# Kernel optimization log

Hardware: AMD Instinct MI355X
Metric: run time of the kernel (lower is better)

## Reference

```python
import jax, jax.numpy as jnp
import numpy as np

N_U, N_I, D_IN_U, D_IN_I, D, D_QOL, B = 4096, 4096, 256, 256, 256, 4, 8192

def _w(key, shape, scale=0.05):
    return (jax.random.normal(key, shape) * scale).astype(jnp.float32)

def setup_inputs() -> dict:
    key = jax.random.key(0)
    ks = jax.random.split(key, 24)
    inp = {
        "x_u": jax.random.normal(ks[0], (N_U, D_IN_U), jnp.float32),
        "x_i": jax.random.normal(ks[1], (N_I, D_IN_I), jnp.float32),
        "social_adj": jax.random.randint(ks[2], (N_U, N_U), 0, 2, jnp.int32),
        "ui_adj": jax.random.randint(ks[3], (N_U, N_I), 0, 2, jnp.int32),
        "user_idx": jax.random.randint(ks[4], (B,), 0, N_U, jnp.int32),
        "item_idx": jax.random.randint(ks[5], (B,), 0, N_I, jnp.int32),
        "q_u": jax.random.normal(ks[6], (N_U, D_QOL), jnp.float32),
        # params (Linear stored as [in, out]; y = x @ W + b)
        "user_W": _w(ks[7], (D_IN_U, D)), "user_b": jnp.zeros((D,), jnp.float32),
        "item_W": _w(ks[8], (D_IN_I, D)), "item_b": jnp.zeros((D,), jnp.float32),
        "soc_W": _w(ks[9], (D, D)), "soc_a": _w(ks[10], (2 * D,)),
        "cnt_W": _w(ks[11], (D, D)), "cnt_a": _w(ks[12], (2 * D,)),
        "gate_W": _w(ks[13], (D_QOL, D)), "gate_b": jnp.zeros((D,), jnp.float32),
        "qproj_W": _w(ks[14], (D_QOL, D)), "qproj_b": jnp.zeros((D,), jnp.float32),
        "alpha_q": jnp.float32(0.3),
        "pred_W1": _w(ks[15], (2 * D, D)), "pred_b1": jnp.zeros((D,), jnp.float32),
        "pred_W2": _w(ks[16], (D, 1)), "pred_b2": jnp.zeros((1,), jnp.float32),
    }
    return inp

def _gat(Wh_src, Wh_dst, a, adj):
    """GAT additive attention: src rows attend over dst cols where adj!=0.
    Rows with no neighbors produce zero output (matches nan_to_num + zeroing)."""
    d = Wh_src.shape[-1]
    a1 = Wh_src @ a[:d]          # [N_src]
    a2 = Wh_dst @ a[d:]          # [N_dst]
    e = jax.nn.leaky_relu(a1[:, None] + a2[None, :], 0.2)  # [N_src, N_dst]
    mask = adj != 0
    neg_inf = jnp.float32(-jnp.inf)
    m = jnp.max(jnp.where(mask, e, neg_inf), axis=-1, keepdims=True)
    m = jnp.where(jnp.isfinite(m), m, 0.0)  # guard empty rows
    ex = jnp.where(mask, jnp.exp(e - m), 0.0)
    denom = jnp.sum(ex, axis=-1, keepdims=True)
    alpha = jnp.where(denom > 0, ex / jnp.where(denom > 0, denom, 1.0), 0.0)
    out = alpha @ Wh_dst
    return out, alpha

def reference(x_u, x_i, social_adj, ui_adj, user_idx, item_idx, q_u,
              user_W, user_b, item_W, item_b, soc_W, soc_a, cnt_W, cnt_a,
              gate_W, gate_b, qproj_W, qproj_b, alpha_q,
              pred_W1, pred_b1, pred_W2, pred_b2):
    h_u = x_u @ user_W + user_b               # [N_u, D]
    h_i = x_i @ item_W + item_b               # [N_i, D]
    # social attention (users over users)
    Wh = h_u @ soc_W
    soc_msg, alpha_s = _gat(Wh, Wh, soc_a, social_adj)
    # content attention (users over items)
    Wu = h_u @ cnt_W
    Wi = h_i @ cnt_W
    cnt_msg, alpha_c = _gat(Wu, Wi, cnt_a, ui_adj)
    h_u_out = jax.nn.elu(soc_msg + cnt_msg + h_u)
    # QoL gate
    gate = jax.nn.sigmoid(q_u @ gate_W + gate_b)
    qproj = q_u @ qproj_W + qproj_b
    h_u_out = h_u_out + alpha_q * gate * qproj
    # pair prediction (dropout inactive at eval)
    cat = jnp.concatenate([h_u_out[user_idx], h_i[item_idx]], axis=-1)  # [B, 2D]
    hid = jax.nn.relu(cat @ pred_W1 + pred_b1)
    r = (hid @ pred_W2 + pred_b2)[..., 0]
    r_hat = 1.0 + 4.0 * jax.nn.sigmoid(r)
    return r_hat, alpha_s, alpha_c
```

## Files before the change

### kernel.cpp

```cpp
#include <hip/hip_runtime.h>

typedef unsigned short u16;
typedef unsigned int u32;
typedef unsigned char u8;
typedef unsigned long long u64;
typedef float f32x4 __attribute__((ext_vector_type(4)));
typedef int i32x4 __attribute__((ext_vector_type(4)));
typedef __bf16 bf16x8 __attribute__((ext_vector_type(8)));

#define NU 4096
#define DD 256
#define BB 8192

__device__ inline u16 f2b(float f) {
    u32 u = __builtin_bit_cast(u32, f);
    u32 r = (u + 0x7fffu + ((u >> 16) & 1u)) >> 16;
    return (u16)r;
}
__device__ inline float b2f(u16 v) { return __builtin_bit_cast(float, (u32)v << 16); }
__device__ inline float lrelu(float x) { return x > 0.f ? x : 0.2f * x; }
__device__ inline float decmax(u32 e) {
    return __builtin_bit_cast(float, (e >> 31) ? (e & 0x7fffffffu) : ~e);
}

#define BARRIER_LGKM() asm volatile("s_waitcnt lgkmcnt(0)\ns_barrier" ::: "memory")

__global__ __launch_bounds__(256) void k_pro(
    const float* __restrict__ x_u, const float* __restrict__ x_i,
    const float* __restrict__ user_W, const float* __restrict__ item_W, const float* __restrict__ pred_W1,
    const float* __restrict__ soc_W, const float* __restrict__ soc_a,
    const float* __restrict__ cnt_W, const float* __restrict__ cnt_a,
    const float* __restrict__ user_b, const float* __restrict__ item_b,
    u16* __restrict__ xu_b, u16* __restrict__ xi_b,
    u16* __restrict__ uWt, u16* __restrict__ iWt, u16* __restrict__ p1Wt,
    float* __restrict__ uvec,
    u16* __restrict__ WusT, u16* __restrict__ WicT,
    float* __restrict__ b_us, float* __restrict__ b_ic, u32* __restrict__ MhEnc) {
    __shared__ float t[64][65];
    __shared__ float sa[256];
    const int b = blockIdx.x;
    const int tid = threadIdx.x;

    if (b < 1024) {
        const float* in = (b < 512) ? x_u : x_i;
        u16* out = (b < 512) ? xu_b : xi_b;
        int i = (b & 511) * 256 + tid;
        const float4 v0 = *(const float4*)(in + (size_t)i * 8);
        const float4 v1 = *(const float4*)(in + (size_t)i * 8 + 4);
        u16 u[8] = {f2b(v0.x), f2b(v0.y), f2b(v0.z), f2b(v0.w),
                    f2b(v1.x), f2b(v1.y), f2b(v1.z), f2b(v1.w)};
        *(uint4*)(out + (size_t)i * 8) = *(uint4*)u;
    } else if (b < 1088) {
        int j = b - 1024;
        const float* in;
        u16* out;
        int R;
        if (j < 16) { in = user_W; out = uWt; R = 256; }
        else if (j < 32) { in = item_W; out = iWt; R = 256; j -= 16; }
        else { in = pred_W1; out = p1Wt; R = 512; j -= 32; }
        int rb = (j >> 2) * 64, cb = (j & 3) * 64;
        for (int k = 0; k < 16; ++k) {
            int idx = k * 256 + tid;
            int lr = idx >> 6, lc = idx & 63;
            t[lr][lc] = in[(size_t)(rb + lr) * 256 + cb + lc];
        }
        __syncthreads();
        for (int k = 0; k < 16; ++k) {
            int idx = k * 256 + tid;
            int lr = idx >> 6, lc = idx & 63;
            out[(size_t)(cb + lr) * R + rb + lc] = f2b(t[lc][lr]);
        }
    } else if (b < 1092) {
        int bb = b - 1088;
        if (bb == 0 && tid < 2) MhEnc[tid] = 0u;
        const float* W = (bb < 2) ? soc_W : cnt_W;
        const float* a = ((bb < 2) ? soc_a : cnt_a) + (bb & 1) * 256;
        int lane = tid & 63, wv = tid >> 6;
        sa[tid] = a[tid];
        __syncthreads();
        for (int rr = 0; rr < 64; ++rr) {
            int in = wv * 64 + rr;
            float4 w4 = *(const float4*)(W + (size_t)in * 256 + lane * 4);
            float acc = w4.x * sa[lane * 4] + w4.y * sa[lane * 4 + 1] + w4.z * sa[lane * 4 + 2] + w4.w * sa[lane * 4 + 3];
#pragma unroll
            for (int off = 32; off; off >>= 1) acc += __shfl_down(acc, off);
            if (lane == 0) uvec[bb * 256 + in] = acc;
        }
    } else {
        int j = b - 1092;
        int p = j >> 4;
        int tile = j & 15;
        const float* A = p ? item_W : user_W;
        const float* Bw = p ? cnt_W : soc_W;
        const float* bvec = p ? item_b : user_b;
        u16* outT = p ? WicT : WusT;
        float* outb = p ? b_ic : b_us;
        int m0 = (tile >> 2) * 64, n0 = (tile & 3) * 64;
        int m = m0 + (tid >> 4) * 4, n = n0 + (tid & 15) * 4;
        float acc[4][4];
#pragma unroll
        for (int i = 0; i < 4; ++i)
#pragma unroll
            for (int k = 0; k < 4; ++k) acc[i][k] = 0.f;
        for (int k0 = 0; k0 < 256; k0 += 4) {
            float aa[4][4], bb2[4][4];
#pragma unroll
            for (int i = 0; i < 4; ++i) {
                float4 v = *(const float4*)(A + (size_t)(m + i) * 256 + k0);
                aa[i][0] = v.x; aa[i][1] = v.y; aa[i][2] = v.z; aa[i][3] = v.w;
            }
#pragma unroll
            for (int k = 0; k < 4; ++k) {
                float4 v = *(const float4*)(Bw + (size_t)(k0 + k) * 256 + n);
                bb2[k][0] = v.x; bb2[k][1] = v.y; bb2[k][2] = v.z; bb2[k][3] = v.w;
            }
#pragma unroll
            for (int i = 0; i < 4; ++i)
#pragma unroll
                for (int k = 0; k < 4; ++k)
#pragma unroll
                    for (int jj = 0; jj < 4; ++jj) acc[i][jj] += aa[i][k] * bb2[k][jj];
        }
#pragma unroll
        for (int i = 0; i < 4; ++i)
#pragma unroll
            for (int jj = 0; jj < 4; ++jj) outT[(size_t)(n + jj) * 256 + m + i] = f2b(acc[i][jj]);
        if (tile >> 2 == 0 && tid < 64) {
            int nn = n0 + tid;
            float s = 0.f;
            for (int k = 0; k < 256; ++k) s += bvec[k] * Bw[(size_t)k * 256 + nn];
            outb[nn] = s;
        }
    }
}

__global__ __launch_bounds__(256) void k_gemm4(
    const u16* __restrict__ xu_b, const u16* __restrict__ xi_b,
    const u16* __restrict__ uWt, const u16* __restrict__ iWt,
    const u16* __restrict__ WusT, const u16* __restrict__ WicT,
    const float* __restrict__ user_b, const float* __restrict__ item_b,
    const float* __restrict__ b_us, const float* __restrict__ b_ic,
    float* __restrict__ h_u_f, float* __restrict__ h_i_f, u16* __restrict__ h_i_b,
    u16* __restrict__ WhT, u16* __restrict__ WiT) {
    const int z = blockIdx.z;
    const int M = 4096, N = 256, K = 256;
    const u16* A = (z == 0 || z == 2) ? xu_b : xi_b;
    const u16* Bt = (z == 0) ? uWt : (z == 1) ? iWt : (z == 2) ? WusT : WicT;
    const float* bias = (z == 0) ? user_b : (z == 1) ? item_b : (z == 2) ? b_us : b_ic;
    float* Cf = (z == 0) ? h_u_f : (z == 1) ? h_i_f : nullptr;
    u16* Cb = (z == 1) ? h_i_b : nullptr;
    u16* Cbt = (z == 2) ? WhT : (z == 3) ? WiT : nullptr;

    __shared__ u16 As[64 * 64];
    __shared__ u16 Bs[64 * 64];
    const int tid = threadIdx.x;
    const int lane = tid & 63, wv = tid >> 6;
    const int bm = blockIdx.x * 64, bn = blockIdx.y * 64;
    const int wm = (wv >> 1) * 32, wn = (wv & 1) * 32;
    f32x4 acc[2][2];
#pragma unroll
    for (int i = 0; i < 2; i++)
#pragma unroll
        for (int j = 0; j < 2; j++) acc[i][j] = f32x4{0.f, 0.f, 0.f, 0.f};

    char* Ab = (char*)As;
    char* Bb = (char*)Bs;
    const int r = tid >> 2;
    const int ib0 = (tid & 3) * 32;
    const int swz = (r & 7) << 4;

    for (int k0 = 0; k0 < K; k0 += 64) {
        const uint4* ga = (const uint4*)(A + (size_t)(bm + r) * K + k0 + (ib0 >> 1));
        const uint4* gb = (const uint4*)(Bt + (size_t)(bn + r) * K + k0 + (ib0 >> 1));
        uint4 va0 = ga[0], va1 = ga[1];
        uint4 vb0 = gb[0], vb1 = gb[1];
        __syncthreads();
        *(uint4*)(Ab + r * 128 + ((ib0) ^ swz)) = va0;
        *(uint4*)(Ab + r * 128 + ((ib0 + 16) ^ swz)) = va1;
        *(uint4*)(Bb + r * 128 + ((ib0) ^ swz)) = vb0;
        *(uint4*)(Bb + r * 128 + ((ib0 + 16) ^ swz)) = vb1;
        __syncthreads();
#pragma unroll
        for (int kh = 0; kh < 2; ++kh) {
            bf16x8 af[2], bfr[2];
#pragma unroll
            for (int mf = 0; mf < 2; ++mf) {
                int row = wm + mf * 16 + (lane & 15);
                int kb = kh * 64 + ((lane >> 4) << 4);
                af[mf] = *(const bf16x8*)(Ab + row * 128 + (kb ^ ((row & 7) << 4)));
            }
#pragma unroll
            for (int nf = 0; nf < 2; ++nf) {
                int row = wn + nf * 16 + (lane & 15);
                int kb = kh * 64 + ((lane >> 4) << 4);
                bfr[nf] = *(const bf16x8*)(Bb + row * 128 + (kb ^ ((row & 7) << 4)));
            }
#pragma unroll
            for (int mf = 0; mf < 2; ++mf)
#pragma unroll
                for (int nf = 0; nf < 2; ++nf)
                    acc[mf][nf] = __builtin_amdgcn_mfma_f32_16x16x32_bf16(af[mf], bfr[nf], acc[mf][nf], 0, 0, 0);
        }
    }
#pragma unroll
    for (int mf = 0; mf < 2; ++mf) {
#pragma unroll
        for (int nf = 0; nf < 2; ++nf) {
            int col = bn + wn + nf * 16 + (lane & 15);
            int row0 = bm + wm + mf * 16 + ((lane >> 4) << 2);
            float bv = bias[col];
            float v[4];
#pragma unroll
            for (int q = 0; q < 4; ++q) {
                float x = acc[mf][nf][q] + bv;
                v[q] = x;
                if (Cf) Cf[(size_t)(row0 + q) * N + col] = x;
                if (Cb) Cb[(size_t)(row0 + q) * N + col] = f2b(x);
            }
            if (Cbt) {
                uint2 p;
                p.x = (u32)f2b(v[0]) | ((u32)f2b(v[1]) << 16);
                p.y = (u32)f2b(v[2]) | ((u32)f2b(v[3]) << 16);
                *(uint2*)(Cbt + (size_t)col * M + row0) = p;
            }
        }
    }
}

__global__ __launch_bounds__(256) void k_gemv_a(const float* __restrict__ h_u, const float* __restrict__ h_i,
                                                const float* __restrict__ uvec, float* __restrict__ avec,
                                                u32* __restrict__ MhEnc) {
    int tid = threadIdx.x, lane = tid & 63, wv = tid >> 6;
    int ib = blockIdx.x * 64;
    const float* H = (wv == 3) ? h_i : h_u;
    const float* u = uvec + wv * 256;
    float4 u4 = *(const float4*)(u + lane * 4);
    float runm = -1e30f;
    for (int rr = 0; rr < 64; ++rr) {
        int row = ib + rr;
        float4 h4 = *(const float4*)(H + (size_t)row * 256 + lane * 4);
        float acc = h4.x * u4.x + h4.y * u4.y + h4.z * u4.z + h4.w * u4.w;
#pragma unroll
        for (int off = 32; off; off >>= 1) acc += __shfl_down(acc, off);
        if (lane == 0) {
            avec[wv * 4096 + row] = acc;
            runm = fmaxf(runm, acc);
        }
    }
    if (lane == 0 && (wv & 1)) {
        u32 b = __builtin_bit_cast(u32, runm);
        u32 e = (b >> 31) ? ~b : (b | 0x80000000u);
        atomicMax(&MhEnc[wv >> 1], e);
    }
}

__global__ __launch_bounds__(512) void k_scan(const int* __restrict__ adjS, const int* __restrict__ adjC,
                                              u8* __restrict__ bits) {
    const int z = blockIdx.z;
    const int* adj = z ? adjC : adjS;
    u8* bz = bits + (size_t)z * 2097152;
    const int lane = threadIdx.x & 63, wv = threadIdx.x >> 6;
    const int row = blockIdx.x * 8 + wv;
    const int* base = adj + (size_t)row * 4096 + lane * 8;
    i32x4 va[8], vb[8];
#pragma unroll
    for (int s = 0; s < 8; ++s) {
        va[s] = __builtin_nontemporal_load((const i32x4*)(base + s * 512));
        vb[s] = __builtin_nontemporal_load((const i32x4*)(base + s * 512 + 4));
    }
    const size_t bo = (size_t)row * 512 + lane;
#pragma unroll
    for (int s = 0; s < 8; ++s) {
        i32x4 v0 = va[s], v1 = vb[s];
        u32 b = (u32)(v0.x != 0) | ((u32)(v0.y != 0) << 1) | ((u32)(v0.z != 0) << 2) | ((u32)(v0.w != 0) << 3) |
                ((u32)(v1.x != 0) << 4) | ((u32)(v1.y != 0) << 5) | ((u32)(v1.z != 0) << 6) | ((u32)(v1.w != 0) << 7);
        bz[bo + s * 64] = (u8)b;
    }
}

__global__ __launch_bounds__(512, 4) void k_pv(const u8* __restrict__ bits,
                                               const float* __restrict__ avec, const u32* __restrict__ MhEnc,
                                               const u16* __restrict__ WhT, const u16* __restrict__ WiT,
                                               float* __restrict__ dpart, u16* __restrict__ msgpart) {
    const int z = blockIdx.z;
    const int ib = blockIdx.x * 64;
    const int jb = blockIdx.y * 512;
    const int tid = threadIdx.x, lane = tid & 63, wv = tid >> 6;
    const u8* bz = bits + (size_t)z * 2097152;
    const float* a1 = avec + z * 8192;
    const float* a2 = a1 + 4096;
    const u16* Pt = z ? WiT : WhT;

    __shared__ float a2s[512];
    __shared__ float s_a1[64], s_mr[64];
    __shared__ u16 Atile[64 * 512];
    char* Ab = (char*)Atile;

    if (tid < 512) a2s[tid] = a2[jb + tid];
    if (tid < 64) {
        float a = a1[ib + tid];
        float mhg = decmax(MhEnc[z]);
        s_a1[tid] = a;
        s_mr[tid] = lrelu(a + mhg);
    }
    __syncthreads();

    const int r0 = wv * 8;
    u8 bvv[8];
    const size_t bo = (size_t)(ib + r0) * 512 + (jb >> 3) + lane;
#pragma unroll
    for (int rr = 0; rr < 8; ++rr) bvv[rr] = bz[bo + (size_t)rr * 512];
    const float4 A0 = *(const float4*)(a2s + lane * 8);
    const float4 A1 = *(const float4*)(a2s + lane * 8 + 4);
    const float av[8] = {A0.x, A0.y, A0.z, A0.w, A1.x, A1.y, A1.z, A1.w};
#pragma unroll
    for (int rr = 0; rr < 8; ++rr) {
        const int r = r0 + rr;
        const float a1r = s_a1[r], mr = s_mr[r];
        const u32 byte = bvv[rr];
        float ex[8];
        float acc = 0.f;
#pragma unroll
        for (int k = 0; k < 8; ++k) {
            float e = __expf(lrelu(a1r + av[k]) - mr);
            ex[k] = ((byte >> k) & 1) ? e : 0.f;
            acc += ex[k];
        }
#pragma unroll
        for (int off = 32; off; off >>= 1) acc += __shfl_down(acc, off);
        if (lane == 0) dpart[((size_t)z * 8 + blockIdx.y) * 4096 + ib + r] = acc;
        u16 pk[8];
#pragma unroll
        for (int k = 0; k < 8; ++k) pk[k] = f2b(ex[k]);
        *(uint4*)(Ab + r * 1024 + ((lane * 16) ^ ((r & 7) << 4))) = *(uint4*)pk;
    }
    BARRIER_LGKM();

    f32x4 acc[4][2];
#pragma unroll
    for (int i = 0; i < 4; i++)
#pragma unroll
        for (int j = 0; j < 2; j++) acc[i][j] = f32x4{0.f, 0.f, 0.f, 0.f};

    const u16* pts = Pt + (size_t)(wv * 32 + (lane & 15)) * 4096 + jb + ((lane >> 4) << 3);
    bf16x8 bcur0 = *(const bf16x8*)(pts);
    bf16x8 bcur1 = *(const bf16x8*)(pts + (size_t)16 * 4096);
    for (int ks = 0; ks < 16; ++ks) {
        bf16x8 bnxt0, bnxt1;
        if (ks < 15) {
            bnxt0 = *(const bf16x8*)(pts + (ks + 1) * 32);
            bnxt1 = *(const bf16x8*)(pts + (size_t)16 * 4096 + (ks + 1) * 32);
        }
#pragma unroll
        for (int mf = 0; mf < 4; ++mf) {
            int ra = mf * 16 + (lane & 15);
            bf16x8 af = *(const bf16x8*)(Ab + ra * 1024 + ((ks * 64 + ((lane >> 4) << 4)) ^ ((ra & 7) << 4)));
            acc[mf][0] = __builtin_amdgcn_mfma_f32_16x16x32_bf16(af, bcur0, acc[mf][0], 0, 0, 0);
            acc[mf][1] = __builtin_amdgcn_mfma_f32_16x16x32_bf16(af, bcur1, acc[mf][1], 0, 0, 0);
        }
        bcur0 = bnxt0;
        bcur1 = bnxt1;
    }

    u16* mp = msgpart + ((size_t)(z * 8 + blockIdx.y) * 4096 + ib) * 256;
#pragma unroll
    for (int mf = 0; mf < 4; ++mf) {
        int rr = mf * 16 + ((lane >> 4) << 2);
#pragma unroll
        for (int nf = 0; nf < 2; ++nf) {
            int col = wv * 32 + nf * 16 + (lane & 15);
#pragma unroll
            for (int q = 0; q < 4; ++q) mp[(size_t)(rr + q) * 256 + col] = f2b(acc[mf][nf][q]);
        }
    }
}

__global__ __launch_bounds__(256) void k_alpha(const u8* __restrict__ bits,
                                               const float* __restrict__ avec, const u32* __restrict__ MhEnc,
                                               const float* __restrict__ dpart, float* __restrict__ out) {
    const int z = blockIdx.z;
    const int ib = blockIdx.x * 16;
    const int tid = threadIdx.x, lane = tid & 63, wv = tid >> 6;
    const u8* bz = bits + (size_t)z * 2097152;
    const float* a1 = avec + z * 8192;
    const float* a2 = a1 + 4096;
    float* alpha = out + 8192 + (size_t)z * 16777216;

    __shared__ float a2s[4096];
    __shared__ u8 bls[16 * 512];
    __shared__ float s_a1[16], s_mr[16], s_inv[16];

#pragma unroll
    for (int k = 0; k < 4; ++k)
        *(float4*)(a2s + (k * 256 + tid) * 4) = *(const float4*)(a2 + (k * 256 + tid) * 4);
#pragma unroll
    for (int k = 0; k < 2; ++k)
        *(uint4*)(bls + (k * 256 + tid) * 16) = *(const uint4*)(bz + (size_t)ib * 512 + (k * 256 + tid) * 16);
    if (tid < 16) {
        float a = a1[ib + tid];
        float mhg = decmax(MhEnc[z]);
        s_a1[tid] = a;
        s_mr[tid] = lrelu(a + mhg);
        float d = 0.f;
#pragma unroll
        for (int s = 0; s < 8; ++s) d += dpart[((size_t)(z * 8 + s)) * 4096 + ib + tid];
        s_inv[tid] = d > 0.f ? 1.f / d : 0.f;
    }
    __syncthreads();

    const int bsub = lane >> 1;
    const int sh = (lane & 1) * 4;
#pragma unroll
    for (int rr = 0; rr < 4; ++rr) {
        const int r = wv * 4 + rr;
        const int row = ib + r;
        const float a1r = s_a1[r], mr = s_mr[r], ivr = s_inv[r];
        float* ap = alpha + (size_t)row * 4096;
        const u8* brow = bls + r * 512;
#pragma unroll
        for (int c = 0; c < 16; ++c) {
            const int col = c * 256 + lane * 4;
            const u32 nib = ((u32)brow[c * 32 + bsub]) >> sh;
            const float4 a4 = *(const float4*)(a2s + col);
            f32x4 o;
            o.x = (nib & 1) ? __expf(lrelu(a1r + a4.x) - mr) * ivr : 0.f;
            o.y = (nib & 2) ? __expf(lrelu(a1r + a4.y) - mr) * ivr : 0.f;
            o.z = (nib & 4) ? __expf(lrelu(a1r + a4.z) - mr) * ivr : 0.f;
            o.w = (nib & 8) ? __expf(lrelu(a1r + a4.w) - mr) * ivr : 0.f;
            __builtin_nontemporal_store(o, (f32x4*)(ap + col));
        }
    }
}

__global__ __launch_bounds__(256) void k_post(const u16* __restrict__ msgpart, const float* __restrict__ dpart,
                                              const float* __restrict__ h_u, const float* __restrict__ q_u,
                                              const float* __restrict__ gate_W, const float* __restrict__ gate_b,
                                              const float* __restrict__ qproj_W, const float* __restrict__ qproj_b,
                                              const float* __restrict__ alpha_q, u16* __restrict__ huo_b) {
    int i = blockIdx.x;
    int n = threadIdx.x;
    __shared__ float red[16];
    if (n < 16) red[n] = dpart[(size_t)n * 4096 + i];
    __syncthreads();
    float d0 = 0.f, d1 = 0.f;
#pragma unroll
    for (int p = 0; p < 8; ++p) { d0 += red[p]; d1 += red[8 + p]; }
    float inv0 = d0 > 0.f ? 1.f / d0 : 0.f;
    float inv1 = d1 > 0.f ? 1.f / d1 : 0.f;
    float s0 = 0.f, s1 = 0.f;
#pragma unroll
    for (int p = 0; p < 8; ++p) {
        s0 += b2f(msgpart[((size_t)p * 4096 + i) * 256 + n]);
        s1 += b2f(msgpart[((size_t)(8 + p) * 4096 + i) * 256 + n]);
    }
    float v = inv0 * s0 + inv1 * s1 + h_u[(size_t)i * 256 + n];
    v = v > 0.f ? v : expm1f(v);
    float q0 = q_u[i * 4 + 0], q1 = q_u[i * 4 + 1], q2 = q_u[i * 4 + 2], q3 = q_u[i * 4 + 3];
    float g = q0 * gate_W[n] + q1 * gate_W[256 + n] + q2 * gate_W[512 + n] + q3 * gate_W[768 + n] + gate_b[n];
    g = 1.f / (1.f + __expf(-g));
    float qp = q0 * qproj_W[n] + q1 * qproj_W[256 + n] + q2 * qproj_W[512 + n] + q3 * qproj_W[768 + n] + qproj_b[n];
    float o = v + alpha_q[0] * g * qp;
    huo_b[(size_t)i * 256 + n] = f2b(o);
}

__global__ __launch_bounds__(512) void k_pred(const u16* __restrict__ huo_b, const u16* __restrict__ h_i_b,
                                              const int* __restrict__ uidx, const int* __restrict__ iidx,
                                              const u16* __restrict__ Bt, const float* __restrict__ b1,
                                              const float* __restrict__ W2, const float* __restrict__ b2,
                                              float* __restrict__ out) {
    __shared__ u16 As[64 * 512];
    __shared__ float redL[512];
    const int tid = threadIdx.x, lane = tid & 63, wv = tid >> 6;
    const int bm = blockIdx.x * 64;
    char* Ab = (char*)As;

    {
        const int r = tid >> 3;
        const int uix = uidx[bm + r], iix = iidx[bm + r];
        const int sswz = (r & 7) << 4;
#pragma unroll
        for (int c = 0; c < 8; ++c) {
            int e = c * 64 + (tid & 7) * 8;
            const u16* src = (e < 256) ? (huo_b + (size_t)uix * 256 + e) : (h_i_b + (size_t)iix * 256 + (e - 256));
            uint4 v = *(const uint4*)src;
            *(uint4*)(Ab + r * 1024 + ((e * 2) ^ sswz)) = v;
        }
    }
    __syncthreads();

    const int n0 = wv * 32;
    f32x4 acc[4][2];
#pragma unroll
    for (int i = 0; i < 4; i++)
#pragma unroll
        for (int j = 0; j < 2; j++) acc[i][j] = f32x4{0.f, 0.f, 0.f, 0.f};

    for (int ks = 0; ks < 16; ++ks) {
        bf16x8 bfr[2];
#pragma unroll
        for (int nf = 0; nf < 2; ++nf)
            bfr[nf] = *(const bf16x8*)(Bt + (size_t)(n0 + nf * 16 + (lane & 15)) * 512 + ks * 32 + ((lane >> 4) << 3));
#pragma unroll
        for (int mf = 0; mf < 4; ++mf) {
            int ra = mf * 16 + (lane & 15);
            bf16x8 af = *(const bf16x8*)(Ab + ra * 1024 + ((ks * 64 + ((lane >> 4) << 4)) ^ ((ra & 7) << 4)));
#pragma unroll
            for (int nf = 0; nf < 2; ++nf)
                acc[mf][nf] = __builtin_amdgcn_mfma_f32_16x16x32_bf16(af, bfr[nf], acc[mf][nf], 0, 0, 0);
        }
    }

    float b1v[2], w2v[2];
#pragma unroll
    for (int nf = 0; nf < 2; ++nf) {
        int col = n0 + nf * 16 + (lane & 15);
        b1v[nf] = b1[col];
        w2v[nf] = W2[col];
    }
#pragma unroll
    for (int mf = 0; mf < 4; ++mf) {
#pragma unroll
        for (int q = 0; q < 4; ++q) {
            float val = 0.f;
#pragma unroll
            for (int nf = 0; nf < 2; ++nf) val += fmaxf(acc[mf][nf][q] + b1v[nf], 0.f) * w2v[nf];
#pragma unroll
            for (int off = 1; off < 16; off <<= 1) val += __shfl_xor(val, off);
            if ((lane & 15) == 0) redL[wv * 64 + mf * 16 + ((lane >> 4) << 2) + q] = val;
        }
    }
    __syncthreads();
    if (tid < 64) {
        float r = b2[0];
#pragma unroll
        for (int w = 0; w < 8; ++w) r += redL[w * 64 + tid];
        out[bm + tid] = 1.f + 4.f / (1.f + __expf(-r));
    }
}

extern "C" void kernel_launch(void* const* d_in, const int* in_sizes, int n_in,
                              void* d_out, int out_size, void* d_ws, size_t ws_size,
                              hipStream_t stream) {
    const float* x_u = (const float*)d_in[0];
    const float* x_i = (const float*)d_in[1];
    const int* adjS = (const int*)d_in[2];
    const int* adjC = (const int*)d_in[3];
    const int* uidx = (const int*)d_in[4];
    const int* iidx = (const int*)d_in[5];
    const float* q_u = (const float*)d_in[6];
    const float* user_W = (const float*)d_in[7];
    const float* user_b = (const float*)d_in[8];
    const float* item_W = (const float*)d_in[9];
    const float* item_b = (const float*)d_in[10];
    const float* soc_W = (const float*)d_in[11];
    const float* soc_a = (const float*)d_in[12];
    const float* cnt_W = (const float*)d_in[13];
    const float* cnt_a = (const float*)d_in[14];
    const float* gate_W = (const float*)d_in[15];
    const float* gate_b = (const float*)d_in[16];
    const float* qproj_W = (const float*)d_in[17];
    const float* qproj_b = (const float*)d_in[18];
    const float* alpha_q = (const float*)d_in[19];
    const float* pred_W1 = (const float*)d_in[20];
    const float* pred_b1 = (const float*)d_in[21];
    const float* pred_W2 = (const float*)d_in[22];
    const float* pred_b2 = (const float*)d_in[23];
    float* out = (float*)d_out;

    char* w = (char*)d_ws;
    size_t off = 0;
    auto alloc = [&](size_t bytes) -> void* {
        void* p = w + off;
        off = (off + bytes + 255) & ~(size_t)255;
        return p;
    };
    u16* xu_b = (u16*)alloc((size_t)NU * DD * 2);
    u16* xi_b = (u16*)alloc((size_t)NU * DD * 2);
    u16* uWt = (u16*)alloc(256 * 256 * 2);
    u16* iWt = (u16*)alloc(256 * 256 * 2);
    u16* p1Wt = (u16*)alloc(512 * 256 * 2);
    u16* WusT = (u16*)alloc(256 * 256 * 2);
    u16* WicT = (u16*)alloc(256 * 256 * 2);
    float* b_us = (float*)alloc(256 * 4);
    float* b_ic = (float*)alloc(256 * 4);
    float* uvec = (float*)alloc(4 * 256 * 4);
    float* h_u_f = (float*)alloc((size_t)NU * DD * 4);
    float* h_i_f = (float*)alloc((size_t)NU * DD * 4);
    u16* h_i_b = (u16*)alloc((size_t)NU * DD * 2);
    u16* WhT = (u16*)alloc((size_t)NU * DD * 2);
    u16* WiT = (u16*)alloc((size_t)NU * DD * 2);
    float* avec = (float*)alloc(4 * 4096 * 4);
    u32* MhEnc = (u32*)alloc(2 * 4);
    float* dpart = (float*)alloc((size_t)2 * 8 * 4096 * 4);
    u8* bits = (u8*)alloc((size_t)2 * 2097152);
    u16* msgpart = (u16*)alloc((size_t)16 * 4096 * 256 * 2);
    u16* huo_b = (u16*)alloc((size_t)NU * DD * 2);
    (void)in_sizes; (void)n_in; (void)out_size; (void)ws_size;

    k_scan<<<dim3(512, 1, 2), 512, 0, stream>>>(adjS, adjC, bits);
    k_pro<<<1124, 256, 0, stream>>>(x_u, x_i, user_W, item_W, pred_W1, soc_W, soc_a, cnt_W, cnt_a,
                                    user_b, item_b, xu_b, xi_b, uWt, iWt, p1Wt, uvec, WusT, WicT,
                                    b_us, b_ic, MhEnc);
    k_gemm4<<<dim3(64, 4, 4), 256, 0, stream>>>(xu_b, xi_b, uWt, iWt, WusT, WicT, user_b, item_b, b_us, b_ic,
                                                h_u_f, h_i_f, h_i_b, WhT, WiT);
    k_gemv_a<<<64, 256, 0, stream>>>(h_u_f, h_i_f, uvec, avec, MhEnc);
    k_pv<<<dim3(64, 8, 2), 512, 0, stream>>>(bits, avec, MhEnc, WhT, WiT, dpart, msgpart);
    k_alpha<<<dim3(256, 1, 2), 256, 0, stream>>>(bits, avec, MhEnc, dpart, out);
    k_post<<<4096, 256, 0, stream>>>(msgpart, dpart, h_u_f, q_u, gate_W, gate_b, qproj_W, qproj_b, alpha_q, huo_b);
    k_pred<<<128, 512, 0, stream>>>(huo_b, h_i_b, uidx, iidx, p1Wt, pred_b1, pred_W2, pred_b2, out);
}
```

Baseline: 192.7 us.

## Fuse adjacency scan with softmax denominator and alpha output writing

Moves the adjacency scan after the attention-logit gemv and fuses it with computing each row's softmax denominator and writing the full alpha matrices. The separate k_alpha kernel and the per-partition denominator buffer in k_pv are removed. This saves a re-read of the bitmask and a kernel launch, and drops the denominator reduction from k_pv. In exchange, each wave computes the exponentials twice per row. The adjacency read no longer overlaps the prologue and GEMM kernels, and the nontemporal load/store hints are dropped.

New measurement: 199.8 us. 1.04x slower.

```diff
diff --git a/kernel.cpp b/kernel.cpp
--- a/kernel.cpp
+++ b/kernel.cpp
@@ -254,34 +254,88 @@
     }
 }
 
-__global__ __launch_bounds__(512) void k_scan(const int* __restrict__ adjS, const int* __restrict__ adjC,
-                                              u8* __restrict__ bits) {
+__global__ __launch_bounds__(512) void k_scanalpha(const int* __restrict__ adjS, const int* __restrict__ adjC,
+                                                   const float* __restrict__ avec, const u32* __restrict__ MhEnc,
+                                                   u8* __restrict__ bits, float* __restrict__ invd,
+                                                   float* __restrict__ out) {
     const int z = blockIdx.z;
     const int* adj = z ? adjC : adjS;
     u8* bz = bits + (size_t)z * 2097152;
-    const int lane = threadIdx.x & 63, wv = threadIdx.x >> 6;
+    const float* a1 = avec + z * 8192;
+    const float* a2 = a1 + 4096;
+    float* alpha = out + 8192 + (size_t)z * 16777216;
+    const int tid = threadIdx.x, lane = tid & 63, wv = tid >> 6;
     const int row = blockIdx.x * 8 + wv;
+
+    __shared__ float a2s[4096];
+#pragma unroll
+    for (int k = 0; k < 2; ++k) {
+        int c = (k * 512 + tid) * 4;
+        *(float4*)(a2s + c) = *(const float4*)(a2 + c);
+    }
+    __syncthreads();
+
+    const float mhg = decmax(MhEnc[z]);
+    const float a1r = a1[row];
+    const float mr = lrelu(a1r + mhg);
+
     const int* base = adj + (size_t)row * 4096 + lane * 8;
     i32x4 va[8], vb[8];
 #pragma unroll
     for (int s = 0; s < 8; ++s) {
-        va[s] = __builtin_nontemporal_load((const i32x4*)(base + s * 512));
-        vb[s] = __builtin_nontemporal_load((const i32x4*)(base + s * 512 + 4));
-    }
-    const size_t bo = (size_t)row * 512 + lane;
+        va[s] = *(const i32x4*)(base + s * 512);
+        vb[s] = *(const i32x4*)(base + s * 512 + 4);
+    }
+    u32 mask8[8];
+    float d = 0.f;
 #pragma unroll
     for (int s = 0; s < 8; ++s) {
         i32x4 v0 = va[s], v1 = vb[s];
-        u32 b = (u32)(v0.x != 0) | ((u32)(v0.y != 0) << 1) | ((u32)(v0.z != 0) << 2) | ((u32)(v0.w != 0) << 3) |
+        u32 m = (u32)(v0.x != 0) | ((u32)(v0.y != 0) << 1) | ((u32)(v0.z != 0) << 2) | ((u32)(v0.w != 0) << 3) |
                 ((u32)(v1.x != 0) << 4) | ((u32)(v1.y != 0) << 5) | ((u32)(v1.z != 0) << 6) | ((u32)(v1.w != 0) << 7);
-        bz[bo + s * 64] = (u8)b;
+        mask8[s] = m;
+        bz[(size_t)row * 512 + s * 64 + lane] = (u8)m;
+        const float4 A0 = *(const float4*)(a2s + s * 512 + lane * 8);
+        const float4 A1 = *(const float4*)(a2s + s * 512 + lane * 8 + 4);
+        d += (m & 1) ? __expf(lrelu(a1r + A0.x) - mr) : 0.f;
+        d += (m & 2) ? __expf(lrelu(a1r + A0.y) - mr) : 0.f;
+        d += (m & 4) ? __expf(lrelu(a1r + A0.z) - mr) : 0.f;
+        d += (m & 8) ? __expf(lrelu(a1r + A0.w) - mr) : 0.f;
+        d += (m & 16) ? __expf(lrelu(a1r + A1.x) - mr) : 0.f;
+        d += (m & 32) ? __expf(lrelu(a1r + A1.y) - mr) : 0.f;
+        d += (m & 64) ? __expf(lrelu(a1r + A1.z) - mr) : 0.f;
+        d += (m & 128) ? __expf(lrelu(a1r + A1.w) - mr) : 0.f;
+    }
+#pragma unroll
+    for (int off = 32; off; off >>= 1) d += __shfl_down(d, off);
+    d = __shfl(d, 0);
+    const float inv = d > 0.f ? 1.f / d : 0.f;
+    if (lane == 0) invd[(size_t)z * 4096 + row] = inv;
+
+    float* ap = alpha + (size_t)row * 4096;
+#pragma unroll
+    for (int s = 0; s < 8; ++s) {
+        const u32 m = mask8[s];
+        const float4 A0 = *(const float4*)(a2s + s * 512 + lane * 8);
+        const float4 A1 = *(const float4*)(a2s + s * 512 + lane * 8 + 4);
+        f32x4 o0, o1;
+        o0.x = (m & 1) ? __expf(lrelu(a1r + A0.x) - mr) * inv : 0.f;
+        o0.y = (m & 2) ? __expf(lrelu(a1r + A0.y) - mr) * inv : 0.f;
+        o0.z = (m & 4) ? __expf(lrelu(a1r + A0.z) - mr) * inv : 0.f;
+        o0.w = (m & 8) ? __expf(lrelu(a1r + A0.w) - mr) * inv : 0.f;
+        o1.x = (m & 16) ? __expf(lrelu(a1r + A1.x) - mr) * inv : 0.f;
+        o1.y = (m & 32) ? __expf(lrelu(a1r + A1.y) - mr) * inv : 0.f;
+        o1.z = (m & 64) ? __expf(lrelu(a1r + A1.z) - mr) * inv : 0.f;
+        o1.w = (m & 128) ? __expf(lrelu(a1r + A1.w) - mr) * inv : 0.f;
+        *(f32x4*)(ap + s * 512 + lane * 8) = o0;
+        *(f32x4*)(ap + s * 512 + lane * 8 + 4) = o1;
     }
 }
 
 __global__ __launch_bounds__(512, 4) void k_pv(const u8* __restrict__ bits,
                                                const float* __restrict__ avec, const u32* __restrict__ MhEnc,
                                                const u16* __restrict__ WhT, const u16* __restrict__ WiT,
-                                               float* __restrict__ dpart, u16* __restrict__ msgpart) {
+                                               u16* __restrict__ msgpart) {
     const int z = blockIdx.z;
     const int ib = blockIdx.x * 64;
     const int jb = blockIdx.y * 512;
@@ -319,16 +373,11 @@
         const float a1r = s_a1[r], mr = s_mr[r];
         const u32 byte = bvv[rr];
         float ex[8];
-        float acc = 0.f;
 #pragma unroll
         for (int k = 0; k < 8; ++k) {
             float e = __expf(lrelu(a1r + av[k]) - mr);
             ex[k] = ((byte >> k) & 1) ? e : 0.f;
-            acc += ex[k];
-        }
-#pragma unroll
-        for (int off = 32; off; off >>= 1) acc += __shfl_down(acc, off);
-        if (lane == 0) dpart[((size_t)z * 8 + blockIdx.y) * 4096 + ib + r] = acc;
+        }
         u16 pk[8];
 #pragma unroll
         for (int k = 0; k < 8; ++k) pk[k] = f2b(ex[k]);
@@ -375,78 +424,15 @@
     }
 }
 
-__global__ __launch_bounds__(256) void k_alpha(const u8* __restrict__ bits,
-                                               const float* __restrict__ avec, const u32* __restrict__ MhEnc,
-                                               const float* __restrict__ dpart, float* __restrict__ out) {
-    const int z = blockIdx.z;
-    const int ib = blockIdx.x * 16;
-    const int tid = threadIdx.x, lane = tid & 63, wv = tid >> 6;
-    const u8* bz = bits + (size_t)z * 2097152;
-    const float* a1 = avec + z * 8192;
-    const float* a2 = a1 + 4096;
-    float* alpha = out + 8192 + (size_t)z * 16777216;
-
-    __shared__ float a2s[4096];
-    __shared__ u8 bls[16 * 512];
-    __shared__ float s_a1[16], s_mr[16], s_inv[16];
-
-#pragma unroll
-    for (int k = 0; k < 4; ++k)
-        *(float4*)(a2s + (k * 256 + tid) * 4) = *(const float4*)(a2 + (k * 256 + tid) * 4);
-#pragma unroll
-    for (int k = 0; k < 2; ++k)
-        *(uint4*)(bls + (k * 256 + tid) * 16) = *(const uint4*)(bz + (size_t)ib * 512 + (k * 256 + tid) * 16);
-    if (tid < 16) {
-        float a = a1[ib + tid];
-        float mhg = decmax(MhEnc[z]);
-        s_a1[tid] = a;
-        s_mr[tid] = lrelu(a + mhg);
-        float d = 0.f;
-#pragma unroll
-        for (int s = 0; s < 8; ++s) d += dpart[((size_t)(z * 8 + s)) * 4096 + ib + tid];
-        s_inv[tid] = d > 0.f ? 1.f / d : 0.f;
-    }
-    __syncthreads();
-
-    const int bsub = lane >> 1;
-    const int sh = (lane & 1) * 4;
-#pragma unroll
-    for (int rr = 0; rr < 4; ++rr) {
-        const int r = wv * 4 + rr;
-        const int row = ib + r;
-        const float a1r = s_a1[r], mr = s_mr[r], ivr = s_inv[r];
-        float* ap = alpha + (size_t)row * 4096;
-        const u8* brow = bls + r * 512;
-#pragma unroll
-        for (int c = 0; c < 16; ++c) {
-            const int col = c * 256 + lane * 4;
-            const u32 nib = ((u32)brow[c * 32 + bsub]) >> sh;
-            const float4 a4 = *(const float4*)(a2s + col);
-            f32x4 o;
-            o.x = (nib & 1) ? __expf(lrelu(a1r + a4.x) - mr) * ivr : 0.f;
-            o.y = (nib & 2) ? __expf(lrelu(a1r + a4.y) - mr) * ivr : 0.f;
-            o.z = (nib & 4) ? __expf(lrelu(a1r + a4.z) - mr) * ivr : 0.f;
-            o.w = (nib & 8) ? __expf(lrelu(a1r + a4.w) - mr) * ivr : 0.f;
-            __builtin_nontemporal_store(o, (f32x4*)(ap + col));
-        }
-    }
-}
-
-__global__ __launch_bounds__(256) void k_post(const u16* __restrict__ msgpart, const float* __restrict__ dpart,
+__global__ __launch_bounds__(256) void k_post(const u16* __restrict__ msgpart, const float* __restrict__ invd,
                                               const float* __restrict__ h_u, const float* __restrict__ q_u,
                                               const float* __restrict__ gate_W, const float* __restrict__ gate_b,
                                               const float* __restrict__ qproj_W, const float* __restrict__ qproj_b,
                                               const float* __restrict__ alpha_q, u16* __restrict__ huo_b) {
     int i = blockIdx.x;
     int n = threadIdx.x;
-    __shared__ float red[16];
-    if (n < 16) red[n] = dpart[(size_t)n * 4096 + i];
-    __syncthreads();
-    float d0 = 0.f, d1 = 0.f;
-#pragma unroll
-    for (int p = 0; p < 8; ++p) { d0 += red[p]; d1 += red[8 + p]; }
-    float inv0 = d0 > 0.f ? 1.f / d0 : 0.f;
-    float inv1 = d1 > 0.f ? 1.f / d1 : 0.f;
+    float inv0 = invd[i];
+    float inv1 = invd[4096 + i];
     float s0 = 0.f, s1 = 0.f;
 #pragma unroll
     for (int p = 0; p < 8; ++p) {
@@ -591,21 +577,20 @@
     u16* WiT = (u16*)alloc((size_t)NU * DD * 2);
     float* avec = (float*)alloc(4 * 4096 * 4);
     u32* MhEnc = (u32*)alloc(2 * 4);
-    float* dpart = (float*)alloc((size_t)2 * 8 * 4096 * 4);
+    float* invd = (float*)alloc((size_t)2 * 4096 * 4);
     u8* bits = (u8*)alloc((size_t)2 * 2097152);
     u16* msgpart = (u16*)alloc((size_t)16 * 4096 * 256 * 2);
     u16* huo_b = (u16*)alloc((size_t)NU * DD * 2);
     (void)in_sizes; (void)n_in; (void)out_size; (void)ws_size;
 
-    k_scan<<<dim3(512, 1, 2), 512, 0, stream>>>(adjS, adjC, bits);
     k_pro<<<1124, 256, 0, stream>>>(x_u, x_i, user_W, item_W, pred_W1, soc_W, soc_a, cnt_W, cnt_a,
                                     user_b, item_b, xu_b, xi_b, uWt, iWt, p1Wt, uvec, WusT, WicT,
                                     b_us, b_ic, MhEnc);
     k_gemm4<<<dim3(64, 4, 4), 256, 0, stream>>>(xu_b, xi_b, uWt, iWt, WusT, WicT, user_b, item_b, b_us, b_ic,
                                                 h_u_f, h_i_f, h_i_b, WhT, WiT);
     k_gemv_a<<<64, 256, 0, stream>>>(h_u_f, h_i_f, uvec, avec, MhEnc);
-    k_pv<<<dim3(64, 8, 2), 512, 0, stream>>>(bits, avec, MhEnc, WhT, WiT, dpart, msgpart);
-    k_alpha<<<dim3(256, 1, 2), 256, 0, stream>>>(bits, avec, MhEnc, dpart, out);
-    k_post<<<4096, 256, 0, stream>>>(msgpart, dpart, h_u_f, q_u, gate_W, gate_b, qproj_W, qproj_b, alpha_q, huo_b);
+    k_scanalpha<<<dim3(512, 1, 2), 512, 0, stream>>>(adjS, adjC, avec, MhEnc, bits, invd, out);
+    k_pv<<<dim3(64, 8, 2), 512, 0, stream>>>(bits, avec, MhEnc, WhT, WiT, msgpart);
+    k_post<<<4096, 256, 0, stream>>>(msgpart, invd, h_u_f, q_u, gate_W, gate_b, qproj_W, qproj_b, alpha_q, huo_b);
     k_pred<<<128, 512, 0, stream>>>(huo_b, h_i_b, uidx, iidx, p1Wt, pred_b1, pred_W2, pred_b2, out);
 }
```
